# Kernel tuning notes

Hardware: AMD Instinct MI355X
Metric: run time of the kernel (lower is better)

Reference implementation:

```python
import jax, jax.numpy as jnp
import numpy as np

# ---- config (from DAREConfig init_kwargs) ----
TAU = 0.1
RHO_VIS = 0.5          # is_visual=True -> rho_target = rho_vis_target
PREFIX_KAPPA = 64
LAMBDA_RATIO = 1.0
LAMBDA_SOFT = 0.1
LAMBDA_HARD = 1.0

B, S = 256, 32768


def setup_inputs() -> dict:
    key = jax.random.key(0)
    k1, k2 = jax.random.split(key)
    importance = jax.random.normal(k1, (B, S), dtype=jnp.float32)
    modality_mask = jax.random.randint(k2, (B, S), 0, 2) > 0  # bool [B,S]
    return {"importance": importance, "modality_mask": modality_mask}


def reference(importance, modality_mask):
    """Vectorized DAREController.route(is_visual=True, training=True).

    The torch loop over batch with data-dependent k is replaced by a
    per-row k-th-largest threshold: for each row, k_b = min(int(rho*|mm_b|),
    |valid_b|); tokens with score >= k_b-th largest valid score are kept
    (this matches DifferentiableTopK's hard mask soft>0.5, i.e. exactly the
    top-k scores, assuming no ties).
    """
    mm = modality_mask.astype(bool)          # [B,S]
    b, s = importance.shape

    target = jnp.clip(mm.sum(axis=1).astype(jnp.float32) * RHO_VIS, 1.0)  # [B]
    prefix = jnp.arange(s) < min(PREFIX_KAPPA, s)                          # [S]
    eff = mm & ~prefix[None, :]                                            # [B,S] routable tokens
    n_valid = eff.sum(axis=1)                                              # [B]
    k = jnp.minimum(target.astype(jnp.int32), n_valid)                     # [B] per-row top-k size

    neg_inf = jnp.float32(-jnp.inf)
    masked = jnp.where(eff, importance, neg_inf)                           # [B,S]
    sorted_desc = -jnp.sort(-masked, axis=1)                               # [B,S]
    idx = jnp.clip(k - 1, 0, s - 1)                                        # [B]
    thresh = jnp.take_along_axis(sorted_desc, idx[:, None], axis=1)        # [B,1]
    hard = masked >= thresh                                                # top-k of valid tokens

    keep_mask = prefix[None, :] | (hard & (k > 0)[:, None])                # [B,S]

    # ---- training / is_visual losses ----
    kept = (keep_mask & mm).sum(axis=1).astype(jnp.float32)
    denom = mm.sum(axis=1).astype(jnp.float32) + 1e-6
    actual_ratio = kept / denom
    loss_ratio = jnp.mean(jnp.abs(actual_ratio - RHO_VIS))                 # F.l1_loss

    dropped = mm & ~keep_mask
    n_drop = dropped.sum()
    drop_mean = jnp.sum(jnp.where(dropped, importance, 0.0)) / jnp.maximum(n_drop, 1).astype(jnp.float32)
    loss_soft = jnp.where(n_drop > 0, drop_mean, 0.0)

    loss_hard = jnp.mean(jnp.clip(RHO_VIS - actual_ratio, 0.0))

    return (keep_mask,
            LAMBDA_RATIO * loss_ratio,
            LAMBDA_SOFT * loss_soft,
            LAMBDA_HARD * loss_hard)
```

## Files before the change

kernel.cpp:

```cpp
#include <hip/hip_runtime.h>


#define NB 256
#define NS 32768
#define KAPPA 64
#define NT 1024
#define V4 (NS / NT / 4)
#define NBIN 2048
#define NSEG 256
#define SEGW (NBIN / NSEG)
#define CAND_CAP 4096

typedef float f32x4 __attribute__((ext_vector_type(4)));
typedef int   i32x4 __attribute__((ext_vector_type(4)));
typedef unsigned int u32;

__device__ __forceinline__ u32 fkey(float f) {
    u32 u = __float_as_uint(f);
    return (u & 0x80000000u) ? ~u : (u | 0x80000000u);
}

__global__ __launch_bounds__(NT) void dare_rows(const float* __restrict__ imp,
                                                const int* __restrict__ mask,
                                                float* __restrict__ keep,
                                                float* __restrict__ stats) {
    __shared__ float K[NS];
    __shared__ u32 hist[NBIN];
    __shared__ u32 cand[CAND_CAP];
    __shared__ u32 bm_eff[NT];
    __shared__ u32 wtot[4];
    __shared__ u32 sh_mm, sh_eff, sh_cand;
    __shared__ u32 sh_b0, sh_rem, sh_thresh;
    __shared__ u32 sh_kept, sh_ndrop;
    __shared__ float sh_dsum;

    const int row = blockIdx.x;
    const int tid = threadIdx.x;
    const int lane = tid & 63;
    const f32x4* rimp4  = (const f32x4*)(imp  + (size_t)row * NS);
    const i32x4* rmask4 = (const i32x4*)(mask + (size_t)row * NS);
    f32x4*       rkeep4 = (f32x4*)      (keep + (size_t)row * NS);

    #pragma unroll
    for (int i = 0; i < V4; i++) {
        const int idx4 = tid + i * NT;
        __builtin_amdgcn_global_load_lds(
            (const __attribute__((address_space(1))) u32*)(&rmask4[idx4]),
            (__attribute__((address_space(3))) u32*)(&K[idx4 * 4]),
            16, 0, 0);
    }
    hist[tid] = 0;
    hist[tid + NT] = 0;
    if (tid == 0) {
        sh_mm = 0; sh_eff = 0; sh_cand = 0;
        sh_b0 = 0; sh_rem = 1; sh_thresh = 0;
        sh_kept = 0; sh_ndrop = 0; sh_dsum = 0.0f;
    }
    __syncthreads();

    const i32x4* Km = (const i32x4*)K;
    u32 mmbits = 0, effbits = 0;
    #pragma unroll
    for (int i = 0; i < V4; i++) {
        const int idx4 = tid + i * NT;
        const i32x4 m = Km[idx4];
        #pragma unroll
        for (int j = 0; j < 4; j++) {
            const int e = i * 4 + j;
            const int col = idx4 * 4 + j;
            const bool mm  = (m[j] != 0);
            const bool eff = mm && (col >= KAPPA);
            mmbits  |= (mm  ? 1u : 0u) << e;
            effbits |= (eff ? 1u : 0u) << e;
        }
    }
    bm_eff[tid] = effbits;
    int mm_local  = __popc(mmbits);
    int eff_local = __popc(effbits);
    #pragma unroll
    for (int off = 32; off; off >>= 1) {
        mm_local  += __shfl_down(mm_local, off);
        eff_local += __shfl_down(eff_local, off);
    }
    if (lane == 0) {
        atomicAdd(&sh_mm,  (u32)mm_local);
        atomicAdd(&sh_eff, (u32)eff_local);
    }
    __syncthreads();

    #pragma unroll
    for (int i = 0; i < V4; i++) {
        const int idx4 = tid + i * NT;
        __builtin_amdgcn_global_load_lds(
            (const __attribute__((address_space(1))) u32*)(&rimp4[idx4]),
            (__attribute__((address_space(3))) u32*)(&K[idx4 * 4]),
            16, 0, 0);
    }
    __syncthreads();

    const f32x4* Kf = (const f32x4*)K;
    #pragma unroll
    for (int i = 0; i < V4; i++) {
        const int idx4 = tid + i * NT;
        const f32x4 v = Kf[idx4];
        #pragma unroll
        for (int j = 0; j < 4; j++) {
            if ((effbits >> (i * 4 + j)) & 1u) atomicAdd(&hist[fkey(v[j]) >> 21], 1u);
        }
    }
    __syncthreads();

    u32 r[SEGW];
    u32 hsum = 0, s = 0;
    if (tid < NSEG) {
        #pragma unroll
        for (int b = 0; b < SEGW; b++) { r[b] = hist[tid * SEGW + b]; hsum += r[b]; }
        s = hsum;
        #pragma unroll
        for (int off = 1; off < 64; off <<= 1) {
            const u32 t = __shfl_down(s, off);
            if (lane + off < 64) s += t;
        }
        if (lane == 0) wtot[tid >> 6] = s;
    }
    __syncthreads();
    if (tid < NSEG) {
        u32 sfull = s;
        for (int w = (tid >> 6) + 1; w < 4; w++) sfull += wtot[w];
        const float target = fmaxf((float)sh_mm * 0.5f, 1.0f);
        const int k = min((int)target, (int)sh_eff);
        const u32 rem = (u32)max(k, 1);
        const u32 above = sfull - hsum;
        if (sfull >= rem && above < rem) {
            u32 cum = above;
            #pragma unroll
            for (int b = SEGW - 1; b >= 0; b--) {
                if (cum + r[b] >= rem) { sh_b0 = tid * SEGW + b; sh_rem = rem - cum; break; }
                cum += r[b];
            }
        }
    }
    __syncthreads();

    const u32 b0 = sh_b0;
    const bool kpos = (sh_eff > 0);
    if (kpos) {
        #pragma unroll
        for (int i = 0; i < V4; i++) {
            const int idx4 = tid + i * NT;
            const f32x4 v = Kf[idx4];
            #pragma unroll
            for (int j = 0; j < 4; j++) {
                if ((effbits >> (i * 4 + j)) & 1u) {
                    const u32 key = fkey(v[j]);
                    if ((key >> 21) == b0) {
                        const u32 pos = atomicAdd(&sh_cand, 1u);
                        if (pos < CAND_CAP) cand[pos] = key;
                    }
                }
            }
        }
    }
    __syncthreads();

    if (tid < 64 && kpos) {
        const u32 total = sh_cand;
        if (total > 0 && total <= CAND_CAP) {
            u32 rem = sh_rem, pref = 0;
            const int slots = (int)((total + 63u) >> 6);
            for (int bit = 20; bit >= 0; bit--) {
                u32 c1 = 0;
                for (int sl = 0; sl < slots; sl++) {
                    const u32 idx = (u32)lane + ((u32)sl << 6);
                    const u32 lw = (idx < total) ? (cand[idx] & 0x1FFFFFu) : 0xFFFFFFFFu;
                    const bool m = (lw >> (bit + 1)) == (pref >> (bit + 1)) && ((lw >> bit) & 1u);
                    c1 += (u32)__popcll(__ballot(m));
                }
                if (c1 >= rem) pref |= 1u << bit; else rem -= c1;
            }
            if (lane == 0) sh_thresh = (b0 << 21) | pref;
        } else if (total > CAND_CAP) {
            u32 rem = sh_rem, pref = 0;
            for (int bit = 20; bit >= 0; bit--) {
                u32 c1 = 0;
                for (int p = lane; p < NS; p += 64) {
                    const int idx4 = p >> 2;
                    const u32 eb = bm_eff[idx4 & (NT - 1)];
                    const int e = ((idx4 >> 10) << 2) | (p & 3);
                    const u32 key = fkey(K[p]);
                    const bool effb = (eb >> e) & 1u;
                    const bool m = effb && ((key >> 21) == b0) &&
                                   ((key & 0x1FFFFFu) >> (bit + 1)) == (pref >> (bit + 1)) &&
                                   ((key >> bit) & 1u);
                    c1 += (u32)__popcll(__ballot(m));
                }
                if (c1 >= rem) pref |= 1u << bit; else rem -= c1;
            }
            if (lane == 0) sh_thresh = (b0 << 21) | pref;
        }
    }
    __syncthreads();

    const u32 thresh = sh_thresh;
    int kept_l = 0, ndrop_l = 0;
    float dsum_l = 0.0f;
    #pragma unroll
    for (int i = 0; i < V4; i++) {
        const int idx4 = tid + i * NT;
        const f32x4 v = Kf[idx4];
        f32x4 o;
        #pragma unroll
        for (int j = 0; j < 4; j++) {
            const int e = i * 4 + j;
            const int col = idx4 * 4 + j;
            const bool mm  = (mmbits >> e) & 1u;
            const bool eff = (effbits >> e) & 1u;
            const bool hard = kpos && eff && (fkey(v[j]) >= thresh);
            const bool kp = (col < KAPPA) || hard;
            o[j] = kp ? 1.0f : 0.0f;
            kept_l += (kp && mm) ? 1 : 0;
            const bool drop = mm && !kp;
            ndrop_l += drop ? 1 : 0;
            dsum_l += drop ? v[j] : 0.0f;
        }
        rkeep4[idx4] = o;
    }
    #pragma unroll
    for (int off = 32; off; off >>= 1) {
        kept_l  += __shfl_down(kept_l, off);
        ndrop_l += __shfl_down(ndrop_l, off);
        dsum_l  += __shfl_down(dsum_l, off);
    }
    if (lane == 0) {
        atomicAdd(&sh_kept,  (u32)kept_l);
        atomicAdd(&sh_ndrop, (u32)ndrop_l);
        atomicAdd(&sh_dsum,  dsum_l);
    }
    __syncthreads();
    if (tid == 0) {
        stats[row * 4 + 0] = (float)sh_kept;
        stats[row * 4 + 1] = (float)sh_mm;
        stats[row * 4 + 2] = (float)sh_ndrop;
        stats[row * 4 + 3] = sh_dsum;
    }
}

__global__ __launch_bounds__(256) void dare_losses(const float* __restrict__ stats,
                                                   float* __restrict__ out) {
    __shared__ float w_a[4], w_h[4], w_n[4], w_d[4];
    const int tid = threadIdx.x;
    const float kept = stats[tid * 4 + 0];
    const float mmc  = stats[tid * 4 + 1];
    const float nd   = stats[tid * 4 + 2];
    const float ds   = stats[tid * 4 + 3];
    const float ratio = kept / (mmc + 1e-6f);
    float a = fabsf(ratio - 0.5f);
    float h = fmaxf(0.5f - ratio, 0.0f);
    float n = nd, d = ds;
    #pragma unroll
    for (int off = 32; off; off >>= 1) {
        a += __shfl_down(a, off);
        h += __shfl_down(h, off);
        n += __shfl_down(n, off);
        d += __shfl_down(d, off);
    }
    const int wid = tid >> 6, lane = tid & 63;
    if (lane == 0) { w_a[wid] = a; w_h[wid] = h; w_n[wid] = n; w_d[wid] = d; }
    __syncthreads();
    if (tid == 0) {
        float sa = 0.f, shh = 0.f, sn = 0.f, sd = 0.f;
        for (int w = 0; w < 4; w++) { sa += w_a[w]; shh += w_h[w]; sn += w_n[w]; sd += w_d[w]; }
        out[0] = sa / (float)NB;
        out[1] = (sn > 0.0f) ? 0.1f * (sd / fmaxf(sn, 1.0f)) : 0.0f;
        out[2] = shh / (float)NB;
    }
}

extern "C" void kernel_launch(void* const* d_in, const int* in_sizes, int n_in,
                              void* d_out, int out_size, void* d_ws, size_t ws_size,
                              hipStream_t stream) {
    const float* imp  = (const float*)d_in[0];
    const int*   mask = (const int*)d_in[1];
    float* out   = (float*)d_out;
    float* stats = (float*)d_ws;

    dare_rows<<<NB, NT, 0, stream>>>(imp, mask, out, stats);
    dare_losses<<<1, 256, 0, stream>>>(stats, out + (size_t)NB * NS);
}
```

Before: 113.6 us.

## Keep importance keys in registers and fuse histogram build with mask scan

Importance values are now loaded straight from global memory into per-thread registers as sortable keys, instead of being staged through a second LDS pass, and the mask is kept alone in shared memory. The histogram build is folded into the mask-bit loop, which removes a barrier and an extra LDS read pass. The overflow fallback changes from a single-wavefront bitwise scan over LDS to a block-wide multi-pass radix histogram over the register keys. The kernel holds 32 keys per thread in registers, which raises register pressure at 1024 threads per block, and float values are rebuilt from keys for the drop sum.

```diff
diff --git a/kernel.cpp b/kernel.cpp
--- a/kernel.cpp
+++ b/kernel.cpp
@@ -20,14 +20,18 @@
     return (u & 0x80000000u) ? ~u : (u | 0x80000000u);
 }
 
+__device__ __forceinline__ float unkey(u32 k) {
+    u32 u = (k & 0x80000000u) ? (k ^ 0x80000000u) : ~k;
+    return __uint_as_float(u);
+}
+
 __global__ __launch_bounds__(NT) void dare_rows(const float* __restrict__ imp,
                                                 const int* __restrict__ mask,
                                                 float* __restrict__ keep,
                                                 float* __restrict__ stats) {
-    __shared__ float K[NS];
+    __shared__ int smask[NS];
     __shared__ u32 hist[NBIN];
     __shared__ u32 cand[CAND_CAP];
-    __shared__ u32 bm_eff[NT];
     __shared__ u32 wtot[4];
     __shared__ u32 sh_mm, sh_eff, sh_cand;
     __shared__ u32 sh_b0, sh_rem, sh_thresh;
@@ -46,7 +50,7 @@
         const int idx4 = tid + i * NT;
         __builtin_amdgcn_global_load_lds(
             (const __attribute__((address_space(1))) u32*)(&rmask4[idx4]),
-            (__attribute__((address_space(3))) u32*)(&K[idx4 * 4]),
+            (__attribute__((address_space(3))) u32*)(&smask[idx4 * 4]),
             16, 0, 0);
     }
     hist[tid] = 0;
@@ -56,9 +60,17 @@
         sh_b0 = 0; sh_rem = 1; sh_thresh = 0;
         sh_kept = 0; sh_ndrop = 0; sh_dsum = 0.0f;
     }
-    __syncthreads();
-
-    const i32x4* Km = (const i32x4*)K;
+
+    u32 keys[V4 * 4];
+    #pragma unroll
+    for (int i = 0; i < V4; i++) {
+        const f32x4 v = rimp4[tid + i * NT];
+        #pragma unroll
+        for (int j = 0; j < 4; j++) keys[i * 4 + j] = fkey(v[j]);
+    }
+    __syncthreads();
+
+    const i32x4* Km = (const i32x4*)smask;
     u32 mmbits = 0, effbits = 0;
     #pragma unroll
     for (int i = 0; i < V4; i++) {
@@ -72,9 +84,9 @@
             const bool eff = mm && (col >= KAPPA);
             mmbits  |= (mm  ? 1u : 0u) << e;
             effbits |= (eff ? 1u : 0u) << e;
-        }
-    }
-    bm_eff[tid] = effbits;
+            if (eff) atomicAdd(&hist[keys[e] >> 21], 1u);
+        }
+    }
     int mm_local  = __popc(mmbits);
     int eff_local = __popc(effbits);
     #pragma unroll
@@ -85,28 +97,6 @@
     if (lane == 0) {
         atomicAdd(&sh_mm,  (u32)mm_local);
         atomicAdd(&sh_eff, (u32)eff_local);
-    }
-    __syncthreads();
-
-    #pragma unroll
-    for (int i = 0; i < V4; i++) {
-        const int idx4 = tid + i * NT;
-        __builtin_amdgcn_global_load_lds(
-            (const __attribute__((address_space(1))) u32*)(&rimp4[idx4]),
-            (__attribute__((address_space(3))) u32*)(&K[idx4 * 4]),
-            16, 0, 0);
-    }
-    __syncthreads();
-
-    const f32x4* Kf = (const f32x4*)K;
-    #pragma unroll
-    for (int i = 0; i < V4; i++) {
-        const int idx4 = tid + i * NT;
-        const f32x4 v = Kf[idx4];
-        #pragma unroll
-        for (int j = 0; j < 4; j++) {
-            if ((effbits >> (i * 4 + j)) & 1u) atomicAdd(&hist[fkey(v[j]) >> 21], 1u);
-        }
     }
     __syncthreads();
 
@@ -146,18 +136,10 @@
     const bool kpos = (sh_eff > 0);
     if (kpos) {
         #pragma unroll
-        for (int i = 0; i < V4; i++) {
-            const int idx4 = tid + i * NT;
-            const f32x4 v = Kf[idx4];
-            #pragma unroll
-            for (int j = 0; j < 4; j++) {
-                if ((effbits >> (i * 4 + j)) & 1u) {
-                    const u32 key = fkey(v[j]);
-                    if ((key >> 21) == b0) {
-                        const u32 pos = atomicAdd(&sh_cand, 1u);
-                        if (pos < CAND_CAP) cand[pos] = key;
-                    }
-                }
+        for (int e = 0; e < V4 * 4; e++) {
+            if (((effbits >> e) & 1u) && ((keys[e] >> 21) == b0)) {
+                const u32 pos = atomicAdd(&sh_cand, 1u);
+                if (pos < CAND_CAP) cand[pos] = keys[e];
             }
         }
     }
@@ -179,25 +161,35 @@
                 if (c1 >= rem) pref |= 1u << bit; else rem -= c1;
             }
             if (lane == 0) sh_thresh = (b0 << 21) | pref;
-        } else if (total > CAND_CAP) {
-            u32 rem = sh_rem, pref = 0;
-            for (int bit = 20; bit >= 0; bit--) {
-                u32 c1 = 0;
-                for (int p = lane; p < NS; p += 64) {
-                    const int idx4 = p >> 2;
-                    const u32 eb = bm_eff[idx4 & (NT - 1)];
-                    const int e = ((idx4 >> 10) << 2) | (p & 3);
-                    const u32 key = fkey(K[p]);
-                    const bool effb = (eb >> e) & 1u;
-                    const bool m = effb && ((key >> 21) == b0) &&
-                                   ((key & 0x1FFFFFu) >> (bit + 1)) == (pref >> (bit + 1)) &&
-                                   ((key >> bit) & 1u);
-                    c1 += (u32)__popcll(__ballot(m));
-                }
-                if (c1 >= rem) pref |= 1u << bit; else rem -= c1;
-            }
-            if (lane == 0) sh_thresh = (b0 << 21) | pref;
-        }
+        }
+    }
+    __syncthreads();
+    if (kpos && sh_cand > CAND_CAP) {
+        u32 pref = b0 << 21, rem = sh_rem;
+        for (int shift = 13; shift >= 0; shift -= 8) {
+            const int width = (shift == 13) ? 8 : ((shift == 5) ? 8 : 5);
+            const int nb = 1 << width;
+            if (tid < 256) hist[tid] = 0;
+            __syncthreads();
+            const u32 himask = ~((1u << (shift + width)) - 1u);
+            #pragma unroll
+            for (int e = 0; e < V4 * 4; e++) {
+                if (((effbits >> e) & 1u) && ((keys[e] & himask) == (pref & himask)))
+                    atomicAdd(&hist[(keys[e] >> shift) & (nb - 1)], 1u);
+            }
+            __syncthreads();
+            if (tid == 0) {
+                u32 rr = rem;
+                int b = nb - 1;
+                for (; b > 0; b--) { const u32 c = hist[b]; if (c >= rr) break; rr -= c; }
+                sh_b0 = (u32)b; sh_rem = rr;
+            }
+            __syncthreads();
+            pref |= sh_b0 << shift;
+            rem = sh_rem;
+            __syncthreads();
+        }
+        if (tid == 0) sh_thresh = pref;
     }
     __syncthreads();
 
@@ -207,7 +199,6 @@
     #pragma unroll
     for (int i = 0; i < V4; i++) {
         const int idx4 = tid + i * NT;
-        const f32x4 v = Kf[idx4];
         f32x4 o;
         #pragma unroll
         for (int j = 0; j < 4; j++) {
@@ -215,13 +206,13 @@
             const int col = idx4 * 4 + j;
             const bool mm  = (mmbits >> e) & 1u;
             const bool eff = (effbits >> e) & 1u;
-            const bool hard = kpos && eff && (fkey(v[j]) >= thresh);
+            const bool hard = kpos && eff && (keys[e] >= thresh);
             const bool kp = (col < KAPPA) || hard;
             o[j] = kp ? 1.0f : 0.0f;
             kept_l += (kp && mm) ? 1 : 0;
             const bool drop = mm && !kp;
             ndrop_l += drop ? 1 : 0;
-            dsum_l += drop ? v[j] : 0.0f;
+            dsum_l += drop ? unkey(keys[e]) : 0.0f;
         }
         rkeep4[idx4] = o;
     }
```

Result: no change. 112.7 us (-0.8%).
